# Performance work log

Hardware: AMD Instinct MI355X
Metric: run time of the kernel (lower is better)

## Reference

```python
import jax, jax.numpy as jnp
import numpy as np

B, T, C, H = 4, 2048, 1024, 16
D = C // H


def setup_inputs() -> dict:
    key = jax.random.key(0)
    ks = jax.random.split(key, 5)
    s = 0.02
    return {
        "x": jax.random.normal(ks[0], (B, T, C), dtype=jnp.float32),
        "W_attn": jax.random.normal(ks[1], (C, 3 * C), dtype=jnp.float32) * s,
        "b_attn": jax.random.normal(ks[2], (3 * C,), dtype=jnp.float32) * s,
        "W_proj": jax.random.normal(ks[3], (C, C), dtype=jnp.float32) * s,
        "b_proj": jax.random.normal(ks[4], (C,), dtype=jnp.float32) * s,
    }


def reference(x, W_attn, b_attn, W_proj, b_proj):
    # QKV projection: [B,T,3C]
    qkv = x @ W_attn + b_attn
    q, k, v = jnp.split(qkv, 3, axis=-1)
    # [B,T,C] -> [B,H,T,D]
    def to_heads(t):
        return t.reshape(B, T, H, D).transpose(0, 2, 1, 3)
    q, k, v = to_heads(q), to_heads(k), to_heads(v)
    scale = 1.0 / np.sqrt(D).astype(np.float32)
    # full (non-causal) attention scores [B,H,T,T]
    att = jnp.einsum("bhqd,bhkd->bhqk", q, k) * scale
    att = jax.nn.softmax(att, axis=-1)
    y = jnp.einsum("bhqk,bhkd->bhqd", att, v)
    y = y.transpose(0, 2, 1, 3).reshape(B, T, C)
    return y @ W_proj + b_proj
```

## Files before the change

kernel.cpp:

```cpp
#include <hip/hip_runtime.h>

#define BATCH 4
#define SEQ   2048
#define CDIM  1024
#define NHEAD 16
#define HDIM  64
#define BH    (BATCH * NHEAD)
#define MROWS (BATCH * SEQ)

typedef __attribute__((ext_vector_type(8))) short  short8;
typedef __attribute__((ext_vector_type(4))) float  floatx4;

#define MFMA_BF16(a, b, c) __builtin_amdgcn_mfma_f32_16x16x32_bf16((a), (b), (c), 0, 0, 0)

#define GLOAD16(g, l) __builtin_amdgcn_global_load_lds( \
    (__attribute__((address_space(1))) void*)(g),       \
    (__attribute__((address_space(3))) void*)(l), 16, 0, 0)

__device__ __forceinline__ unsigned short f2bf(float f) {
    union { float f; unsigned u; } v; v.f = f;
    unsigned u = v.u;
    return (unsigned short)((u + 0x7FFFu + ((u >> 16) & 1u)) >> 16);
}

__device__ __forceinline__ float fast_exp2(float x) {
#if __has_builtin(__builtin_amdgcn_exp2f)
    return __builtin_amdgcn_exp2f(x);
#else
    return exp2f(x);
#endif
}

__device__ __forceinline__ unsigned pack_bf16_trunc(float a, float b) {
    union { float f; unsigned u; } ua, ub;
    ua.f = a; ub.f = b;
    return __builtin_amdgcn_perm(ub.u, ua.u, 0x07060302u);
}

__global__ __launch_bounds__(256) void conv_bf16_kernel(
    const float* __restrict__ in, unsigned short* __restrict__ out)
{
    int i = (blockIdx.x * 256 + threadIdx.x) * 4;
    float4 v = *(const float4*)(in + i);
    ushort4 o;
    o.x = f2bf(v.x); o.y = f2bf(v.y); o.z = f2bf(v.z); o.w = f2bf(v.w);
    *(ushort4*)(out + i) = o;
}

__global__ __launch_bounds__(256) void conv_wt_kernel(
    const float* __restrict__ in, unsigned short* __restrict__ out, int K, int N)
{
    __shared__ float T[64][68];
    const int k0 = blockIdx.y * 64, n0 = blockIdx.x * 64;
    const int tid = threadIdx.x;
    const int r = tid >> 4, c4 = (tid & 15) * 4;
    #pragma unroll
    for (int i = 0; i < 4; ++i) {
        int row = r + i * 16;
        float4 v = *(const float4*)(in + (size_t)(k0 + row) * N + n0 + c4);
        T[row][c4 + 0] = v.x; T[row][c4 + 1] = v.y;
        T[row][c4 + 2] = v.z; T[row][c4 + 3] = v.w;
    }
    __syncthreads();
    #pragma unroll
    for (int i = 0; i < 4; ++i) {
        int nrow = r + i * 16;
        ushort4 o;
        o.x = f2bf(T[c4 + 0][nrow]); o.y = f2bf(T[c4 + 1][nrow]);
        o.z = f2bf(T[c4 + 2][nrow]); o.w = f2bf(T[c4 + 3][nrow]);
        *(ushort4*)(out + (size_t)(n0 + nrow) * K + k0 + c4) = o;
    }
}

__global__ __launch_bounds__(256) void qkv_mfma_kernel(
    const unsigned short* __restrict__ A,
    const unsigned short* __restrict__ Bt,
    const float* __restrict__ bias,
    unsigned short* __restrict__ Qo,
    unsigned short* __restrict__ Ko,
    unsigned short* __restrict__ Vo)
{
    const int K = CDIM;
    __shared__ __align__(16) unsigned short As[128 * 32];
    __shared__ __align__(16) unsigned short Bs[128 * 32];

    const int tid = threadIdx.x;
    const int m0 = blockIdx.y * 128, n0 = blockIdx.x * 128;
    const int w = tid >> 6, lane = tid & 63;
    const int wm = (w >> 1) * 64, wn = (w & 1) * 64;
    const int lm = lane & 15, kg = lane >> 4;

    floatx4 acc[4][4];
    const floatx4 zf = {0.f, 0.f, 0.f, 0.f};
    #pragma unroll
    for (int mt = 0; mt < 4; ++mt)
        #pragma unroll
        for (int nt = 0; nt < 4; ++nt) acc[mt][nt] = zf;

    #pragma unroll 1
    for (int k0 = 0; k0 < K; k0 += 32) {
        __syncthreads();
        #pragma unroll
        for (int i = 0; i < 2; ++i) {
            int ci = i * 256 + tid;
            GLOAD16(A  + (size_t)(m0 + (ci >> 2)) * K + k0 + (ci & 3) * 8, As + ci * 8);
            GLOAD16(Bt + (size_t)(n0 + (ci >> 2)) * K + k0 + (ci & 3) * 8, Bs + ci * 8);
        }
        __syncthreads();
        short8 af[4], bf[4];
        #pragma unroll
        for (int t = 0; t < 4; ++t) {
            af[t] = *(const short8*)(As + (wm + t * 16 + lm) * 32 + kg * 8);
            bf[t] = *(const short8*)(Bs + (wn + t * 16 + lm) * 32 + kg * 8);
        }
        #pragma unroll
        for (int mt = 0; mt < 4; ++mt)
            #pragma unroll
            for (int nt = 0; nt < 4; ++nt)
                acc[mt][nt] = MFMA_BF16(af[mt], bf[nt], acc[mt][nt]);
    }

    #pragma unroll
    for (int nt = 0; nt < 4; ++nt) {
        int col = n0 + wn + nt * 16 + lm;
        float bv = bias[col];
        int which = col >> 10;
        int c1 = col & 1023;
        int h = c1 >> 6, d = c1 & 63;
        #pragma unroll
        for (int mt = 0; mt < 4; ++mt) {
            int mbase = m0 + wm + mt * 16 + kg * 4;
            int b = mbase >> 11;
            int t = mbase & 2047;
            int bh = b * NHEAD + h;
            if (which == 2) {
                ushort4 o;
                o.x = f2bf(acc[mt][nt][0] + bv);
                o.y = f2bf(acc[mt][nt][1] + bv);
                o.z = f2bf(acc[mt][nt][2] + bv);
                o.w = f2bf(acc[mt][nt][3] + bv);
                *(ushort4*)(Vo + ((size_t)bh * 64 + d) * SEQ + t) = o;
            } else {
                unsigned short* dst = (which == 0) ? Qo : Ko;
                float qs = (which == 0) ? 0.18033688011112042f : 1.0f;
                #pragma unroll
                for (int r = 0; r < 4; ++r)
                    dst[((size_t)bh * SEQ + t + r) * 64 + d] =
                        f2bf((acc[mt][nt][r] + bv) * qs);
            }
        }
    }
}

__global__ __launch_bounds__(256) void proj_mfma_kernel(
    const unsigned short* __restrict__ A,
    const unsigned short* __restrict__ Bt,
    const float* __restrict__ bias,
    float* __restrict__ out)
{
    const int K = CDIM;
    __shared__ __align__(16) unsigned short As[128 * 32];
    __shared__ __align__(16) unsigned short Bs[128 * 32];

    const int tid = threadIdx.x;
    const int m0 = blockIdx.y * 128, n0 = blockIdx.x * 128;
    const int w = tid >> 6, lane = tid & 63;
    const int wm = (w >> 1) * 64, wn = (w & 1) * 64;
    const int lm = lane & 15, kg = lane >> 4;

    floatx4 acc[4][4];
    const floatx4 zf = {0.f, 0.f, 0.f, 0.f};
    #pragma unroll
    for (int mt = 0; mt < 4; ++mt)
        #pragma unroll
        for (int nt = 0; nt < 4; ++nt) acc[mt][nt] = zf;

    #pragma unroll 1
    for (int k0 = 0; k0 < K; k0 += 32) {
        __syncthreads();
        #pragma unroll
        for (int i = 0; i < 2; ++i) {
            int ci = i * 256 + tid;
            GLOAD16(A  + (size_t)(m0 + (ci >> 2)) * K + k0 + (ci & 3) * 8, As + ci * 8);
            GLOAD16(Bt + (size_t)(n0 + (ci >> 2)) * K + k0 + (ci & 3) * 8, Bs + ci * 8);
        }
        __syncthreads();
        short8 af[4], bf[4];
        #pragma unroll
        for (int t = 0; t < 4; ++t) {
            af[t] = *(const short8*)(As + (wm + t * 16 + lm) * 32 + kg * 8);
            bf[t] = *(const short8*)(Bs + (wn + t * 16 + lm) * 32 + kg * 8);
        }
        #pragma unroll
        for (int mt = 0; mt < 4; ++mt)
            #pragma unroll
            for (int nt = 0; nt < 4; ++nt)
                acc[mt][nt] = MFMA_BF16(af[mt], bf[nt], acc[mt][nt]);
    }

    #pragma unroll
    for (int nt = 0; nt < 4; ++nt) {
        int col = n0 + wn + nt * 16 + lm;
        float bv = bias[col];
        #pragma unroll
        for (int mt = 0; mt < 4; ++mt) {
            int mbase = m0 + wm + mt * 16 + kg * 4;
            #pragma unroll
            for (int r = 0; r < 4; ++r)
                out[(size_t)(mbase + r) * CDIM + col] = acc[mt][nt][r] + bv;
        }
    }
}

#define PSTR 72

__global__ __launch_bounds__(256) void attn_mfma_kernel(
    const unsigned short* __restrict__ Qg,
    const unsigned short* __restrict__ Kg,
    const unsigned short* __restrict__ Vg,
    unsigned short* __restrict__ Y)
{
    __shared__ __align__(16) unsigned short Ks[64 * PSTR];
    __shared__ __align__(16) unsigned short Vs[64 * PSTR];

    const int tid = threadIdx.x, w = tid >> 6, lane = tid & 63;
    const int lm = lane & 15, kg = lane >> 4;
    const int qb = blockIdx.x, bh = blockIdx.y;
    const size_t base = (size_t)bh * SEQ * 64;

    short8 qf[4][2];
    #pragma unroll
    for (int nt = 0; nt < 4; ++nt)
        #pragma unroll
        for (int c = 0; c < 2; ++c)
            qf[nt][c] = *(const short8*)(
                Qg + base + (size_t)(qb * 256 + w * 64 + nt * 16 + lm) * 64 + c * 32 + kg * 8);

    const floatx4 zf = {0.f, 0.f, 0.f, 0.f};
    floatx4 O[4][4];
    #pragma unroll
    for (int nt = 0; nt < 4; ++nt)
        #pragma unroll
        for (int nd = 0; nd < 4; ++nd) O[nt][nd] = zf;
    float lsum[4] = {0.f, 0.f, 0.f, 0.f};

    #pragma unroll 1
    for (int kb = 0; kb < SEQ / 64; ++kb) {
        __syncthreads();
        #pragma unroll
        for (int i = 0; i < 2; ++i) {
            int lin = i * 256 + tid;
            int row = lin >> 3;
            int c8  = (lin & 7) * 8;
            uint4 kv = *(const uint4*)(Kg + base + (size_t)(kb * 64 + row) * 64 + c8);
            int k2 = row & 31;
            int srow = (row & 32) + ((k2 >> 2) & 1) * 16 + ((k2 >> 3) << 2) + (k2 & 3);
            *(uint4*)(Ks + srow * PSTR + c8) = kv;
            uint4 vv = *(const uint4*)(Vg + base + (size_t)row * SEQ + kb * 64 + c8);
            *(uint4*)(Vs + row * PSTR + c8) = vv;
        }
        __syncthreads();

        #pragma unroll
        for (int ch = 0; ch < 2; ++ch) {
            uint4 pa[4];
            #pragma unroll
            for (int mt = 0; mt < 2; ++mt) {
                floatx4 st[4];
                #pragma unroll
                for (int nt = 0; nt < 4; ++nt) st[nt] = zf;
                #pragma unroll
                for (int c = 0; c < 2; ++c) {
                    short8 kf = *(const short8*)(
                        Ks + (ch * 32 + mt * 16 + lm) * PSTR + c * 32 + kg * 8);
                    #pragma unroll
                    for (int nt = 0; nt < 4; ++nt)
                        st[nt] = MFMA_BF16(kf, qf[nt][c], st[nt]);
                }
                #pragma unroll
                for (int nt = 0; nt < 4; ++nt) {
                    float e0 = fast_exp2(st[nt][0]);
                    float e1 = fast_exp2(st[nt][1]);
                    float e2 = fast_exp2(st[nt][2]);
                    float e3 = fast_exp2(st[nt][3]);
                    lsum[nt] += (e0 + e1) + (e2 + e3);
                    if (mt == 0) {
                        pa[nt].x = pack_bf16_trunc(e0, e1);
                        pa[nt].y = pack_bf16_trunc(e2, e3);
                    } else {
                        pa[nt].z = pack_bf16_trunc(e0, e1);
                        pa[nt].w = pack_bf16_trunc(e2, e3);
                    }
                }
            }
            #pragma unroll
            for (int nd = 0; nd < 4; ++nd) {
                short8 vb = *(const short8*)(
                    Vs + (nd * 16 + lm) * PSTR + ch * 32 + kg * 8);
                #pragma unroll
                for (int nt = 0; nt < 4; ++nt) {
                    short8 paf;
                    __builtin_memcpy(&paf, &pa[nt], 16);
                    O[nt][nd] = MFMA_BF16(paf, vb, O[nt][nd]);
                }
            }
        }
    }

    #pragma unroll
    for (int nt = 0; nt < 4; ++nt) {
        lsum[nt] += __shfl_xor(lsum[nt], 16);
        lsum[nt] += __shfl_xor(lsum[nt], 32);
    }
    float linv[4][4];
    #pragma unroll
    for (int mq = 0; mq < 4; ++mq)
        #pragma unroll
        for (int r = 0; r < 4; ++r)
            linv[mq][r] = 1.0f / __shfl(lsum[mq], kg * 4 + r);

    const int b = bh >> 4, h = bh & 15;
    #pragma unroll
    for (int mq = 0; mq < 4; ++mq)
        #pragma unroll
        for (int r = 0; r < 4; ++r) {
            int t = qb * 256 + w * 64 + mq * 16 + kg * 4 + r;
            #pragma unroll
            for (int nd = 0; nd < 4; ++nd)
                Y[((size_t)(b * SEQ + t)) * CDIM + h * 64 + nd * 16 + lm] =
                    f2bf(O[mq][nd][r] * linv[mq][r]);
        }
}

extern "C" void kernel_launch(void* const* d_in, const int* in_sizes, int n_in,
                              void* d_out, int out_size, void* d_ws, size_t ws_size,
                              hipStream_t stream) {
    const float* x      = (const float*)d_in[0];
    const float* W_attn = (const float*)d_in[1];
    const float* b_attn = (const float*)d_in[2];
    const float* W_proj = (const float*)d_in[3];
    const float* b_proj = (const float*)d_in[4];
    float* out = (float*)d_out;

    char* ws = (char*)d_ws;
    unsigned short* xb  = (unsigned short*)(ws);
    unsigned short* Wat = (unsigned short*)(ws + (size_t)16777216);
    unsigned short* Wpt = (unsigned short*)(ws + (size_t)23068672);
    unsigned short* Qb  = (unsigned short*)(ws + (size_t)25165824);
    unsigned short* Kb  = (unsigned short*)(ws + (size_t)41943040);
    unsigned short* Vtb = (unsigned short*)(ws + (size_t)58720256);
    unsigned short* Yb  = (unsigned short*)(ws + (size_t)75497472);

    conv_bf16_kernel<<<dim3(MROWS * CDIM / 1024), 256, 0, stream>>>(x, xb);
    conv_wt_kernel<<<dim3(3 * CDIM / 64, CDIM / 64), 256, 0, stream>>>(
        W_attn, Wat, CDIM, 3 * CDIM);
    conv_wt_kernel<<<dim3(CDIM / 64, CDIM / 64), 256, 0, stream>>>(
        W_proj, Wpt, CDIM, CDIM);

    qkv_mfma_kernel<<<dim3(3 * CDIM / 128, MROWS / 128), 256, 0, stream>>>(
        xb, Wat, b_attn, Qb, Kb, Vtb);

    attn_mfma_kernel<<<dim3(SEQ / 256, BH), 256, 0, stream>>>(Qb, Kb, Vtb, Yb);

    proj_mfma_kernel<<<dim3(CDIM / 128, MROWS / 128), 256, 0, stream>>>(
        Yb, Wpt, b_proj, out);
}
```

Measured before the change: 329.8 us.

## Double-buffer attention K/V tiles with async global-to-LDS loads and XOR swizzle

The attention kernel now stages K and V tiles directly into LDS with global_load_lds and keeps two buffers, so the load for the next key block is issued before computing the current one. This removes the register round trip and the second barrier per iteration, and lets global loads overlap with MFMA work. The padded LDS layout is replaced by an unpadded one with an XOR chunk swizzle to avoid bank conflicts, and the K row permutation is recomputed to match. It doubles LDS use per block, which may lower occupancy, and correctness depends on the barrier also waiting for the outstanding async loads.

After: 294.3 us. -10.8%, faster.

```diff
diff --git a/kernel.cpp b/kernel.cpp
--- a/kernel.cpp
+++ b/kernel.cpp
@@ -212,7 +212,27 @@
     }
 }
 
-#define PSTR 72
+#define BUFSH 8192
+
+__device__ __forceinline__ void attn_stage_tile(
+    const unsigned short* __restrict__ Kg,
+    const unsigned short* __restrict__ Vg,
+    size_t base, int kb, unsigned short* buf, int tid)
+{
+    unsigned short* Kb_ = buf;
+    unsigned short* Vb_ = buf + 4096;
+    #pragma unroll
+    for (int i = 0; i < 2; ++i) {
+        int lin = i * 256 + tid;
+        int srow = lin >> 3;
+        int chunk = lin & 7;
+        int s2 = srow & 31;
+        int grow = (srow & 32) + ((s2 >> 2) & 3) * 8 + ((s2 >> 4) & 1) * 4 + (s2 & 3);
+        int gch = chunk ^ (srow & 7);
+        GLOAD16(Kg + base + (size_t)(kb * 64 + grow) * 64 + gch * 8, Kb_ + lin * 8);
+        GLOAD16(Vg + base + (size_t)srow * SEQ + kb * 64 + gch * 8, Vb_ + lin * 8);
+    }
+}
 
 __global__ __launch_bounds__(256) void attn_mfma_kernel(
     const unsigned short* __restrict__ Qg,
@@ -220,8 +240,7 @@
     const unsigned short* __restrict__ Vg,
     unsigned short* __restrict__ Y)
 {
-    __shared__ __align__(16) unsigned short Ks[64 * PSTR];
-    __shared__ __align__(16) unsigned short Vs[64 * PSTR];
+    __shared__ __align__(16) unsigned short Smem[2 * BUFSH];
 
     const int tid = threadIdx.x, w = tid >> 6, lane = tid & 63;
     const int lm = lane & 15, kg = lane >> 4;
@@ -244,22 +263,17 @@
         for (int nd = 0; nd < 4; ++nd) O[nt][nd] = zf;
     float lsum[4] = {0.f, 0.f, 0.f, 0.f};
 
+    attn_stage_tile(Kg, Vg, base, 0, Smem, tid);
+
     #pragma unroll 1
     for (int kb = 0; kb < SEQ / 64; ++kb) {
         __syncthreads();
-        #pragma unroll
-        for (int i = 0; i < 2; ++i) {
-            int lin = i * 256 + tid;
-            int row = lin >> 3;
-            int c8  = (lin & 7) * 8;
-            uint4 kv = *(const uint4*)(Kg + base + (size_t)(kb * 64 + row) * 64 + c8);
-            int k2 = row & 31;
-            int srow = (row & 32) + ((k2 >> 2) & 1) * 16 + ((k2 >> 3) << 2) + (k2 & 3);
-            *(uint4*)(Ks + srow * PSTR + c8) = kv;
-            uint4 vv = *(const uint4*)(Vg + base + (size_t)row * SEQ + kb * 64 + c8);
-            *(uint4*)(Vs + row * PSTR + c8) = vv;
-        }
-        __syncthreads();
+        if (kb + 1 < SEQ / 64)
+            attn_stage_tile(Kg, Vg, base, kb + 1, Smem + ((kb + 1) & 1) * BUFSH, tid);
+
+        const unsigned short* Ksb = Smem + (kb & 1) * BUFSH;
+        const unsigned short* Vsb = Ksb + 4096;
+        const int sw = (lm & 7);
 
         #pragma unroll
         for (int ch = 0; ch < 2; ++ch) {
@@ -272,7 +286,7 @@
                 #pragma unroll
                 for (int c = 0; c < 2; ++c) {
                     short8 kf = *(const short8*)(
-                        Ks + (ch * 32 + mt * 16 + lm) * PSTR + c * 32 + kg * 8);
+                        Ksb + (ch * 32 + mt * 16 + lm) * 64 + ((c * 4 + kg) ^ sw) * 8);
                     #pragma unroll
                     for (int nt = 0; nt < 4; ++nt)
                         st[nt] = MFMA_BF16(kf, qf[nt][c], st[nt]);
@@ -296,7 +310,7 @@
             #pragma unroll
             for (int nd = 0; nd < 4; ++nd) {
                 short8 vb = *(const short8*)(
-                    Vs + (nd * 16 + lm) * PSTR + ch * 32 + kg * 8);
+                    Vsb + (nd * 16 + lm) * 64 + ((ch * 4 + kg) ^ sw) * 8);
                 #pragma unroll
                 for (int nt = 0; nt < 4; ++nt) {
                     short8 paf;
```
